# Optimization experiments

Measured on AMD Instinct MI355X. Metric: run time of the kernel, lower is better.

Reference implementation:

```python
import jax, jax.numpy as jnp
import numpy as np

B, C, H, W = 8, 64, 128, 128
O, KS, STRIDE, PAD = 64, 3, 1, 1
K = KS * KS


def setup_inputs() -> dict:
    key = jax.random.key(0)
    k1, k2, k3 = jax.random.split(key, 3)
    x = jax.random.normal(k1, (B, C, H, W), dtype=jnp.float32)
    offset = jax.random.normal(k2, (B, 2 * K, H, W), dtype=jnp.float32)
    weight = jax.random.normal(k3, (O, C, KS, KS), dtype=jnp.float32)
    bias = jnp.zeros((O,), dtype=jnp.float32)
    return {"x": x, "offset": offset, "weight": weight, "bias": bias}


def _deform_conv(x, offset, weight, bias, ks=KS, stride=STRIDE, pad=PAD):
    Bx, Cx, Hx, Wx = x.shape
    Kk = ks * ks
    Ho = (Hx + 2 * pad - ks) // stride + 1
    Wo = (Wx + 2 * pad - ks) // stride + 1
    x_pad = jnp.pad(x, ((0, 0), (0, 0), (pad, pad), (pad, pad)))
    Hp, Wp = Hx + 2 * pad, Wx + 2 * pad
    # base grid (top-left tap, padded coords) -- matches torch code exactly
    ys = jnp.arange(Ho, dtype=x.dtype) * stride
    xs = jnp.arange(Wo, dtype=x.dtype) * stride
    off = offset.reshape(Bx, Kk, 2, Ho, Wo).astype(x.dtype)
    gx = off[:, :, 0] + xs[None, None, None, :]   # [B,K,Ho,Wo]
    gy = off[:, :, 1] + ys[None, None, :, None]
    # bilinear sample with zeros padding (grid_sample align_corners=True round-trips
    # normalization exactly, so we sample at (gy,gx) directly)
    x0 = jnp.floor(gx); y0 = jnp.floor(gy)
    wx1 = gx - x0; wx0 = 1.0 - wx1
    wy1 = gy - y0; wy0 = 1.0 - wy1
    x_flat = x_pad.reshape(Bx, Cx, Hp * Wp)

    def gather(yi, xi, w):
        valid = (xi >= 0) & (xi <= Wp - 1) & (yi >= 0) & (yi <= Hp - 1)
        xi_c = jnp.clip(xi, 0, Wp - 1).astype(jnp.int32)
        yi_c = jnp.clip(yi, 0, Hp - 1).astype(jnp.int32)
        idx = (yi_c * Wp + xi_c).reshape(Bx, -1)           # [B, K*Ho*Wo]
        g = jnp.take_along_axis(x_flat, idx[:, None, :], axis=2)  # [B,C,K*Ho*Wo]
        wv = (w * valid.astype(x.dtype)).reshape(Bx, 1, -1)
        return g * wv

    acc = (gather(y0, x0, wy0 * wx0)
           + gather(y0, x0 + 1.0, wy0 * wx1)
           + gather(y0 + 1.0, x0, wy1 * wx0)
           + gather(y0 + 1.0, x0 + 1.0, wy1 * wx1))
    # channel layout after torch.cat over k: index = k*C + c (k-major)
    sampled = acc.reshape(Bx, Cx, Kk, Ho, Wo).transpose(0, 2, 1, 3, 4)
    sampled = sampled.reshape(Bx, Kk * Cx, Ho, Wo)
    # torch flattens weight as (c, kh, kw) -> index = c*K + k; faithful mismatch
    w_flat = weight.reshape(weight.shape[0], -1).astype(sampled.dtype)  # [O, C*K]
    out = jnp.einsum('oi,bihw->bohw', w_flat, sampled)
    return out + bias[None, :, None, None]


def reference(x, offset, weight, bias):
    return _deform_conv(x, offset, weight, bias)
```

## Files before the change

### kernel.cpp

```cpp
#include <hip/hip_runtime.h>
#include <hip/hip_bf16.h>

#define BB 8
#define CC 64
#define OO 64
#define HH 128
#define WWI 128
#define HWSZ (HH * WWI)
#define KK 9
#define II (KK * CC)

#define PXW 16
#define PYH 16
#define WNX 24
#define WNY 24
#define WROWS (WNX * WNY)

typedef __attribute__((ext_vector_type(8))) _Float16 half8;
typedef __attribute__((ext_vector_type(2))) _Float16 h2;
typedef __attribute__((ext_vector_type(4))) float f32x4;
typedef __attribute__((ext_vector_type(4))) unsigned int uint4v;

__device__ __forceinline__ int iclamp(int v, int lo, int hi) {
    return v < lo ? lo : (v > hi ? hi : v);
}
__device__ __forceinline__ unsigned short f2h(float f) {
    union { _Float16 h; unsigned short s; } v;
    v.h = (_Float16)f;
    return v.s;
}
__device__ __forceinline__ h2 u2h(unsigned u) {
    union { unsigned u; h2 h; } v;
    v.u = u;
    return v.h;
}

__global__ __launch_bounds__(256) void prep_xt(const float* __restrict__ x,
                                               unsigned short* __restrict__ xt) {
    __shared__ float tile[64][65];
    const int blk = blockIdx.x;
    const int b = blk & 7;
    const int p0 = (blk >> 3) * 64;
    const int t = threadIdx.x;
    const int a = t >> 6;
    const int q = t & 63;
    const float* xb = x + (size_t)b * CC * HWSZ + p0;
#pragma unroll
    for (int r = 0; r < 16; ++r) {
        int c = r * 4 + a;
        tile[c][q] = xb[(size_t)c * HWSZ + q];
    }
    __syncthreads();
    unsigned short* xo = xt + ((size_t)b * HWSZ + p0) * CC;
#pragma unroll
    for (int r = 0; r < 16; ++r) {
        int pl = r * 4 + a;
        xo[(size_t)pl * CC + q] = f2h(tile[q][pl]);
    }
}

__global__ void prep_waf(const float* __restrict__ w, unsigned short* __restrict__ waf) {
    int tid = blockIdx.x * 256 + threadIdx.x;
    if (tid < 72 * 512) {
        int slab = tid >> 9;
        int r = tid & 511;
        int l = r >> 3, j = r & 7;
        int m = slab & 3;
        int kc = (slab >> 2) & 1;
        int k = slab >> 3;
        int o = m * 16 + (l & 15);
        int i = k * 64 + kc * 32 + (l >> 4) * 8 + j;
        waf[tid] = f2h(w[(size_t)o * II + i]);
    }
}

__global__ __launch_bounds__(512, 2) void deform_mfma9(
        const unsigned short* __restrict__ xt,
        const float* __restrict__ off,
        const unsigned short* __restrict__ waf,
        const float* __restrict__ bias,
        float* __restrict__ out) {
    extern __shared__ unsigned short win[];

    const int blk = blockIdx.x;
    const int b = blk & 7;
    const int pidx = blk >> 3;
    const int y0 = (pidx >> 3) * PYH;
    const int x0 = (pidx & 7) * PXW;
    const int xleft = x0 - 4, ytop = y0 - 4;

    const int t = threadIdx.x;
    const int wave = t >> 6;
    const int lane = t & 63;
    const int fm = lane & 15;
    const int hi = lane >> 4;
    const int c0s = hi * 8;
    const int c1s = 32 + hi * 8;

    const unsigned short* xtb = xt + (size_t)b * HWSZ * CC;
    const float* offpx = off + (size_t)b * 2 * KK * HWSZ
                             + (size_t)(y0 + wave * 2) * WWI + x0 + fm;

    float ox[3][2], oy[3][2];
#pragma unroll
    for (int k = 0; k < 2; ++k) {
#pragma unroll
        for (int nt = 0; nt < 2; ++nt) {
            ox[k][nt] = offpx[(size_t)(2 * k + 0) * HWSZ + nt * WWI];
            oy[k][nt] = offpx[(size_t)(2 * k + 1) * HWSZ + nt * WWI];
        }
    }

    {
        const int tch = t & 7;
        const int rb = t >> 3;
#pragma unroll
        for (int sw = 0; sw < 9; ++sw) {
            const int r = sw * 64 + rb;
            const int wy = r / WNX, wx = r - wy * WNX;
            const int cy = ytop + wy, cx = xleft + wx;
            if (((unsigned)cy < (unsigned)HH) && ((unsigned)cx < (unsigned)WWI)) {
                const uint4v v = *(const uint4v*)(xtb + (size_t)(cy * WWI + cx) * CC + tch * 8);
                *(uint4v*)&win[r * CC + ((tch ^ (r & 7)) << 3)] = v;
            }
        }
    }
    __syncthreads();

    f32x4 acc[2][4];
#pragma unroll
    for (int nt = 0; nt < 2; ++nt)
#pragma unroll
        for (int m = 0; m < 4; ++m) acc[nt][m] = (f32x4)(0.0f);

    uint4v cb[2][8];
    float  cw[2][4];
    bool   inwf[2];
    int    gidx[2][4];
    half8  afb[2][8];

#define LDSRD(r, kc) (*(const uint4v*)&win[(r) * CC + ((((hi) + ((kc) << 2)) ^ ((r) & 7)) << 3)])

#define ISSUE(u) do {                                                           \
        if ((((u) & 1) == 0) && (((u) >> 1) + 2 < KK)) {                        \
            _Pragma("unroll")                                                   \
            for (int nt = 0; nt < 2; ++nt) {                                    \
                ox[(((u) >> 1) + 2) % 3][nt] =                                  \
                    offpx[(size_t)(2 * (((u) >> 1) + 2) + 0) * HWSZ + nt * WWI];\
                oy[(((u) >> 1) + 2) % 3][nt] =                                  \
                    offpx[(size_t)(2 * (((u) >> 1) + 2) + 1) * HWSZ + nt * WWI];\
            }                                                                   \
        }                                                                       \
        if (((u) & 1) == 0) {                                                   \
            const unsigned short* wk = waf + (size_t)((u) >> 1) * 8 * 512 + lane * 8; \
            _Pragma("unroll")                                                   \
            for (int q = 0; q < 8; ++q)                                         \
                afb[((u) >> 1) & 1][q] = *(const half8*)(wk + (size_t)q * 512); \
        }                                                                       \
        const float gx = ox[((u) >> 1) % 3][(u) & 1] + (float)(x0 + fm);        \
        const float gy = oy[((u) >> 1) % 3][(u) & 1] + (float)(y0 + wave * 2 + ((u) & 1)); \
        const float fxf = floorf(gx), fyf = floorf(gy);                         \
        const float fx = gx - fxf, fy = gy - fyf;                               \
        const int ux0 = (int)fxf - 1, ux1 = (int)fxf;                           \
        const int uy0 = (int)fyf - 1, uy1 = (int)fyf;                           \
        const float vx0 = ((unsigned)ux0 < (unsigned)WWI) ? 1.0f : 0.0f;        \
        const float vx1 = ((unsigned)ux1 < (unsigned)WWI) ? 1.0f : 0.0f;        \
        const float vy0 = ((unsigned)uy0 < (unsigned)HH) ? 1.0f : 0.0f;         \
        const float vy1 = ((unsigned)uy1 < (unsigned)HH) ? 1.0f : 0.0f;         \
        cw[(u) & 1][0] = (1.0f - fy) * (1.0f - fx) * vy0 * vx0;                 \
        cw[(u) & 1][1] = (1.0f - fy) * fx          * vy0 * vx1;                 \
        cw[(u) & 1][2] = fy          * (1.0f - fx) * vy1 * vx0;                 \
        cw[(u) & 1][3] = fy          * fx          * vy1 * vx1;                 \
        const int cx0 = iclamp(ux0, 0, WWI - 1), cx1 = iclamp(ux1, 0, WWI - 1); \
        const int cy0 = iclamp(uy0, 0, HH - 1),  cy1 = iclamp(uy1, 0, HH - 1);  \
        inwf[(u) & 1] = (cx0 >= xleft) & (cx1 <= xleft + WNX - 1)               \
                      & (cy0 >= ytop) & (cy1 <= ytop + WNY - 1);                \
        gidx[(u) & 1][0] = cy0 * WWI + cx0;  gidx[(u) & 1][1] = cy0 * WWI + cx1;\
        gidx[(u) & 1][2] = cy1 * WWI + cx0;  gidx[(u) & 1][3] = cy1 * WWI + cx1;\
        const int wx0 = iclamp(cx0 - xleft, 0, WNX - 1);                        \
        const int wx1 = iclamp(cx1 - xleft, 0, WNX - 1);                        \
        const int wy0 = iclamp(cy0 - ytop, 0, WNY - 1);                         \
        const int wy1 = iclamp(cy1 - ytop, 0, WNY - 1);                         \
        const int r00 = wy0 * WNX + wx0, r01 = wy0 * WNX + wx1;                 \
        const int r10 = wy1 * WNX + wx0, r11 = wy1 * WNX + wx1;                 \
        cb[(u) & 1][0] = LDSRD(r00, 0);  cb[(u) & 1][1] = LDSRD(r00, 1);        \
        cb[(u) & 1][2] = LDSRD(r01, 0);  cb[(u) & 1][3] = LDSRD(r01, 1);        \
        cb[(u) & 1][4] = LDSRD(r10, 0);  cb[(u) & 1][5] = LDSRD(r10, 1);        \
        cb[(u) & 1][6] = LDSRD(r11, 0);  cb[(u) & 1][7] = LDSRD(r11, 1);        \
    } while (0)

#define PROC(u) do {                                                            \
        asm volatile("" : "+v"(cb[(u) & 1][0]), "+v"(cb[(u) & 1][1]),           \
                          "+v"(cb[(u) & 1][2]), "+v"(cb[(u) & 1][3]),           \
                          "+v"(cb[(u) & 1][4]), "+v"(cb[(u) & 1][5]),           \
                          "+v"(cb[(u) & 1][6]), "+v"(cb[(u) & 1][7]));          \
        uint4v A0 = cb[(u) & 1][0], A1 = cb[(u) & 1][1];                        \
        uint4v B0 = cb[(u) & 1][2], B1 = cb[(u) & 1][3];                        \
        uint4v C0 = cb[(u) & 1][4], C1 = cb[(u) & 1][5];                        \
        uint4v D0 = cb[(u) & 1][6], D1 = cb[(u) & 1][7];                        \
        if (!inwf[(u) & 1]) {                                                   \
            const unsigned short* g00 = xtb + (size_t)gidx[(u) & 1][0] * CC;    \
            const unsigned short* g01 = xtb + (size_t)gidx[(u) & 1][1] * CC;    \
            const unsigned short* g10 = xtb + (size_t)gidx[(u) & 1][2] * CC;    \
            const unsigned short* g11 = xtb + (size_t)gidx[(u) & 1][3] * CC;    \
            A0 = *(const uint4v*)(g00 + c0s);  A1 = *(const uint4v*)(g00 + c1s);\
            B0 = *(const uint4v*)(g01 + c0s);  B1 = *(const uint4v*)(g01 + c1s);\
            C0 = *(const uint4v*)(g10 + c0s);  C1 = *(const uint4v*)(g10 + c1s);\
            D0 = *(const uint4v*)(g11 + c0s);  D1 = *(const uint4v*)(g11 + c1s);\
        }                                                                       \
        const _Float16 hw00 = (_Float16)cw[(u) & 1][0];                         \
        const _Float16 hw01 = (_Float16)cw[(u) & 1][1];                         \
        const _Float16 hw10 = (_Float16)cw[(u) & 1][2];                         \
        const _Float16 hw11 = (_Float16)cw[(u) & 1][3];                         \
        const h2 w00v = {hw00, hw00}, w01v = {hw01, hw01};                      \
        const h2 w10v = {hw10, hw10}, w11v = {hw11, hw11};                      \
        half8 bf0, bf1;                                                         \
        h2* rp0 = (h2*)&bf0;                                                    \
        h2* rp1 = (h2*)&bf1;                                                    \
        _Pragma("unroll")                                                       \
        for (int i = 0; i < 4; ++i) {                                           \
            h2 r0 = u2h(A0[i]) * w00v;                                          \
            r0 += u2h(B0[i]) * w01v;                                            \
            r0 += u2h(C0[i]) * w10v;                                            \
            r0 += u2h(D0[i]) * w11v;                                            \
            rp0[i] = r0;                                                        \
            h2 r1 = u2h(A1[i]) * w00v;                                          \
            r1 += u2h(B1[i]) * w01v;                                            \
            r1 += u2h(C1[i]) * w10v;                                            \
            r1 += u2h(D1[i]) * w11v;                                            \
            rp1[i] = r1;                                                        \
        }                                                                       \
        _Pragma("unroll")                                                       \
        for (int m = 0; m < 4; ++m)                                             \
            acc[(u) & 1][m] = __builtin_amdgcn_mfma_f32_16x16x32_f16(           \
                afb[((u) >> 1) & 1][m], bf0, acc[(u) & 1][m], 0, 0, 0);         \
        _Pragma("unroll")                                                       \
        for (int m = 0; m < 4; ++m)                                             \
            acc[(u) & 1][m] = __builtin_amdgcn_mfma_f32_16x16x32_f16(           \
                afb[((u) >> 1) & 1][4 + m], bf1, acc[(u) & 1][m], 0, 0, 0);     \
    } while (0)

    ISSUE(0);  ISSUE(1);
    PROC(0);   ISSUE(2);
    PROC(1);   ISSUE(3);
    PROC(2);   ISSUE(4);
    PROC(3);   ISSUE(5);
    PROC(4);   ISSUE(6);
    PROC(5);   ISSUE(7);
    PROC(6);   ISSUE(8);
    PROC(7);   ISSUE(9);
    PROC(8);   ISSUE(10);
    PROC(9);   ISSUE(11);
    PROC(10);  ISSUE(12);
    PROC(11);  ISSUE(13);
    PROC(12);  ISSUE(14);
    PROC(13);  ISSUE(15);
    PROC(14);  ISSUE(16);
    PROC(15);  ISSUE(17);
    PROC(16);
    PROC(17);

#undef ISSUE
#undef PROC
#undef LDSRD

#pragma unroll
    for (int nt = 0; nt < 2; ++nt) {
        float* outb = out + (size_t)b * OO * HWSZ
                          + (size_t)(y0 + wave * 2 + nt) * WWI + x0 + fm;
#pragma unroll
        for (int m = 0; m < 4; ++m) {
            const int ob = m * 16 + hi * 4;
            const float4 bs = *(const float4*)(bias + ob);
#pragma unroll
            for (int j = 0; j < 4; ++j) {
                outb[(size_t)(ob + j) * HWSZ] = acc[nt][m][j] + ((const float*)&bs)[j];
            }
        }
    }
}

__global__ __launch_bounds__(256) void deform_conv_fallback(
        const float* __restrict__ x, const float* __restrict__ off,
        const float* __restrict__ wmat, const float* __restrict__ bias,
        float* __restrict__ out) {
    const int b = blockIdx.y;
    const int p = blockIdx.x * 256 + threadIdx.x;
    const int wo = p & (WWI - 1);
    const int ho = p >> 7;
    const float* xb = x + (size_t)b * CC * HWSZ;
    const float* offb = off + (size_t)b * 2 * KK * HWSZ + p;
    float acc[OO];
#pragma unroll
    for (int o = 0; o < OO; ++o) acc[o] = 0.0f;
#pragma unroll 1
    for (int k = 0; k < KK; ++k) {
        const float gx = offb[(size_t)(2 * k + 0) * HWSZ] + (float)wo;
        const float gy = offb[(size_t)(2 * k + 1) * HWSZ] + (float)ho;
        const float fxf = floorf(gx), fyf = floorf(gy);
        const float fx = gx - fxf, fy = gy - fyf;
        const int ux0 = (int)fxf - 1, ux1 = (int)fxf;
        const int uy0 = (int)fyf - 1, uy1 = (int)fyf;
        const float vx0 = ((unsigned)ux0 < (unsigned)WWI) ? 1.0f : 0.0f;
        const float vx1 = ((unsigned)ux1 < (unsigned)WWI) ? 1.0f : 0.0f;
        const float vy0 = ((unsigned)uy0 < (unsigned)HH) ? 1.0f : 0.0f;
        const float vy1 = ((unsigned)uy1 < (unsigned)HH) ? 1.0f : 0.0f;
        const float w00 = (1.0f - fy) * (1.0f - fx) * vy0 * vx0;
        const float w01 = (1.0f - fy) * fx * vy0 * vx1;
        const float w10 = fy * (1.0f - fx) * vy1 * vx0;
        const float w11 = fy * fx * vy1 * vx1;
        const int cx0 = iclamp(ux0, 0, WWI - 1), cx1 = iclamp(ux1, 0, WWI - 1);
        const int cy0 = iclamp(uy0, 0, HH - 1), cy1 = iclamp(uy1, 0, HH - 1);
        const int i00 = cy0 * WWI + cx0, i01 = cy0 * WWI + cx1;
        const int i10 = cy1 * WWI + cx0, i11 = cy1 * WWI + cx1;
#pragma unroll 4
        for (int c = 0; c < CC; ++c) {
            const float* xc = xb + (size_t)c * HWSZ;
            const float v = w00 * xc[i00] + w01 * xc[i01] + w10 * xc[i10] + w11 * xc[i11];
            const float* wrow = wmat + (size_t)(k * CC + c);
#pragma unroll
            for (int o = 0; o < OO; ++o) acc[o] = fmaf(wrow[(size_t)o * II], v, acc[o]);
        }
    }
    float* outb = out + (size_t)b * OO * HWSZ + p;
#pragma unroll
    for (int o = 0; o < OO; ++o) outb[(size_t)o * HWSZ] = acc[o] + bias[o];
}

extern "C" void kernel_launch(void* const* d_in, const int* in_sizes, int n_in,
                              void* d_out, int out_size, void* d_ws, size_t ws_size,
                              hipStream_t stream) {
    const float* x    = (const float*)d_in[0];
    const float* off  = (const float*)d_in[1];
    const float* w    = (const float*)d_in[2];
    const float* bias = (const float*)d_in[3];
    float* out = (float*)d_out;

    const size_t xt_bytes  = (size_t)BB * HWSZ * CC * sizeof(unsigned short);
    const size_t waf_bytes = (size_t)72 * 512 * sizeof(unsigned short);

    if (ws_size >= xt_bytes + waf_bytes) {
        unsigned short* xt  = (unsigned short*)d_ws;
        unsigned short* wfp = (unsigned short*)((char*)d_ws + xt_bytes);
        prep_xt<<<dim3((HWSZ / 64) * BB), 256, 0, stream>>>(x, xt);
        prep_waf<<<(72 * 512 + 255) / 256, 256, 0, stream>>>(w, wfp);
        deform_mfma9<<<dim3(BB * (HH / PYH) * (WWI / PXW)), dim3(512),
                       WROWS * CC * sizeof(unsigned short), stream>>>(
            xt, off, wfp, bias, out);
    } else {
        deform_conv_fallback<<<dim3(HWSZ / 256, BB), 256, 0, stream>>>(x, off, w, bias, out);
    }
}
```

Measured before the change: 46.54 us.

## Fuse NCHW-to-NHWC fp16 transpose into main kernel window load

Removes the separate prep_xt pass that transposed x into channel-last fp16 and instead has the main kernel read NCHW fp32 rows directly, converting to fp16 and scattering into the swizzled LDS window. Out-of-window fallback gathers now read eight strided fp32 channels per vector instead of one contiguous fp16 vector. This drops a full read/write pass over x and one kernel launch, but the window is now filled with scalar 2-byte LDS stores and halo tiles read fp32 data (twice the bytes) with overlapping reads between neighbouring tiles.

```diff
diff --git a/kernel.cpp b/kernel.cpp
--- a/kernel.cpp
+++ b/kernel.cpp
@@ -1,5 +1,4 @@
 #include <hip/hip_runtime.h>
-#include <hip/hip_bf16.h>
 
 #define BB 8
 #define CC 64
@@ -33,30 +32,6 @@
     union { unsigned u; h2 h; } v;
     v.u = u;
     return v.h;
-}
-
-__global__ __launch_bounds__(256) void prep_xt(const float* __restrict__ x,
-                                               unsigned short* __restrict__ xt) {
-    __shared__ float tile[64][65];
-    const int blk = blockIdx.x;
-    const int b = blk & 7;
-    const int p0 = (blk >> 3) * 64;
-    const int t = threadIdx.x;
-    const int a = t >> 6;
-    const int q = t & 63;
-    const float* xb = x + (size_t)b * CC * HWSZ + p0;
-#pragma unroll
-    for (int r = 0; r < 16; ++r) {
-        int c = r * 4 + a;
-        tile[c][q] = xb[(size_t)c * HWSZ + q];
-    }
-    __syncthreads();
-    unsigned short* xo = xt + ((size_t)b * HWSZ + p0) * CC;
-#pragma unroll
-    for (int r = 0; r < 16; ++r) {
-        int pl = r * 4 + a;
-        xo[(size_t)pl * CC + q] = f2h(tile[q][pl]);
-    }
 }
 
 __global__ void prep_waf(const float* __restrict__ w, unsigned short* __restrict__ waf) {
@@ -74,8 +49,8 @@
     }
 }
 
-__global__ __launch_bounds__(512, 2) void deform_mfma9(
-        const unsigned short* __restrict__ xt,
+__global__ __launch_bounds__(512, 2) void deform_mfma12(
+        const float* __restrict__ x,
         const float* __restrict__ off,
         const unsigned short* __restrict__ waf,
         const float* __restrict__ bias,
@@ -97,7 +72,7 @@
     const int c0s = hi * 8;
     const int c1s = 32 + hi * 8;
 
-    const unsigned short* xtb = xt + (size_t)b * HWSZ * CC;
+    const float* xb = x + (size_t)b * CC * HWSZ;
     const float* offpx = off + (size_t)b * 2 * KK * HWSZ
                              + (size_t)(y0 + wave * 2) * WWI + x0 + fm;
 
@@ -112,16 +87,30 @@
     }
 
     {
-        const int tch = t & 7;
-        const int rb = t >> 3;
-#pragma unroll
-        for (int sw = 0; sw < 9; ++sw) {
-            const int r = sw * 64 + rb;
-            const int wy = r / WNX, wx = r - wy * WNX;
-            const int cy = ytop + wy, cx = xleft + wx;
-            if (((unsigned)cy < (unsigned)HH) && ((unsigned)cx < (unsigned)WWI)) {
-                const uint4v v = *(const uint4v*)(xtb + (size_t)(cy * WWI + cx) * CC + tch * 8);
-                *(uint4v*)&win[r * CC + ((tch ^ (r & 7)) << 3)] = v;
+#pragma unroll
+        for (int i = 0; i < 3; ++i) {
+            const int task = t + i * 512;
+            const int c  = task & 63;
+            const int wy = task >> 6;
+            const int cy = ytop + wy;
+            if ((unsigned)cy < (unsigned)HH) {
+                const float* src = xb + (size_t)c * HWSZ + (size_t)cy * WWI;
+                const int chunk = c >> 3;
+                const int cin = c & 7;
+#pragma unroll
+                for (int g = 0; g < 6; ++g) {
+                    const int cx = xleft + g * 4;
+                    if ((unsigned)cx < (unsigned)(WWI - 3)) {
+                        const float4 v = *(const float4*)(src + cx);
+                        const int rbase = wy * WNX + (cx - xleft);
+#pragma unroll
+                        for (int e = 0; e < 4; ++e) {
+                            const int r = rbase + e;
+                            win[r * CC + ((chunk ^ (r & 7)) << 3) + cin] =
+                                f2h(((const float*)&v)[e]);
+                        }
+                    }
+                }
             }
         }
     }
@@ -189,6 +178,19 @@
         cb[(u) & 1][6] = LDSRD(r11, 0);  cb[(u) & 1][7] = LDSRD(r11, 1);        \
     } while (0)
 
+#define FBK(dst, gi, cbase) do {                                                \
+        const float* xg_ = xb + (size_t)(gi);                                   \
+        uint4v tmp_;                                                            \
+        _Pragma("unroll")                                                       \
+        for (int jj = 0; jj < 4; ++jj) {                                        \
+            union { h2 h; unsigned u; } pp_;                                    \
+            pp_.h = (h2){(_Float16)xg_[(size_t)((cbase) + 2 * jj) * HWSZ],      \
+                         (_Float16)xg_[(size_t)((cbase) + 2 * jj + 1) * HWSZ]}; \
+            tmp_[jj] = pp_.u;                                                   \
+        }                                                                       \
+        (dst) = tmp_;                                                           \
+    } while (0)
+
 #define PROC(u) do {                                                            \
         asm volatile("" : "+v"(cb[(u) & 1][0]), "+v"(cb[(u) & 1][1]),           \
                           "+v"(cb[(u) & 1][2]), "+v"(cb[(u) & 1][3]),           \
@@ -199,14 +201,10 @@
         uint4v C0 = cb[(u) & 1][4], C1 = cb[(u) & 1][5];                        \
         uint4v D0 = cb[(u) & 1][6], D1 = cb[(u) & 1][7];                        \
         if (!inwf[(u) & 1]) {                                                   \
-            const unsigned short* g00 = xtb + (size_t)gidx[(u) & 1][0] * CC;    \
-            const unsigned short* g01 = xtb + (size_t)gidx[(u) & 1][1] * CC;    \
-            const unsigned short* g10 = xtb + (size_t)gidx[(u) & 1][2] * CC;    \
-            const unsigned short* g11 = xtb + (size_t)gidx[(u) & 1][3] * CC;    \
-            A0 = *(const uint4v*)(g00 + c0s);  A1 = *(const uint4v*)(g00 + c1s);\
-            B0 = *(const uint4v*)(g01 + c0s);  B1 = *(const uint4v*)(g01 + c1s);\
-            C0 = *(const uint4v*)(g10 + c0s);  C1 = *(const uint4v*)(g10 + c1s);\
-            D0 = *(const uint4v*)(g11 + c0s);  D1 = *(const uint4v*)(g11 + c1s);\
+            FBK(A0, gidx[(u) & 1][0], c0s);  FBK(A1, gidx[(u) & 1][0], c1s);    \
+            FBK(B0, gidx[(u) & 1][1], c0s);  FBK(B1, gidx[(u) & 1][1], c1s);    \
+            FBK(C0, gidx[(u) & 1][2], c0s);  FBK(C1, gidx[(u) & 1][2], c1s);    \
+            FBK(D0, gidx[(u) & 1][3], c0s);  FBK(D1, gidx[(u) & 1][3], c1s);    \
         }                                                                       \
         const _Float16 hw00 = (_Float16)cw[(u) & 1][0];                         \
         const _Float16 hw01 = (_Float16)cw[(u) & 1][1];                         \
@@ -262,6 +260,7 @@
 
 #undef ISSUE
 #undef PROC
+#undef FBK
 #undef LDSRD
 
 #pragma unroll
@@ -336,17 +335,14 @@
     const float* bias = (const float*)d_in[3];
     float* out = (float*)d_out;
 
-    const size_t xt_bytes  = (size_t)BB * HWSZ * CC * sizeof(unsigned short);
     const size_t waf_bytes = (size_t)72 * 512 * sizeof(unsigned short);
 
-    if (ws_size >= xt_bytes + waf_bytes) {
-        unsigned short* xt  = (unsigned short*)d_ws;
-        unsigned short* wfp = (unsigned short*)((char*)d_ws + xt_bytes);
-        prep_xt<<<dim3((HWSZ / 64) * BB), 256, 0, stream>>>(x, xt);
+    if (ws_size >= waf_bytes) {
+        unsigned short* wfp = (unsigned short*)d_ws;
         prep_waf<<<(72 * 512 + 255) / 256, 256, 0, stream>>>(w, wfp);
-        deform_mfma9<<<dim3(BB * (HH / PYH) * (WWI / PXW)), dim3(512),
-                       WROWS * CC * sizeof(unsigned short), stream>>>(
-            xt, off, wfp, bias, out);
+        deform_mfma12<<<dim3(BB * (HH / PYH) * (WWI / PXW)), dim3(512),
+                        WROWS * CC * sizeof(unsigned short), stream>>>(
+            x, off, wfp, bias, out);
     } else {
         deform_conv_fallback<<<dim3(HWSZ / 256, BB), 256, 0, stream>>>(x, off, w, bias, out);
     }
```

Result: slower. 50.40 us (+8.3%).
